# Kernel optimization log

Measured on AMD Instinct MI355X. Metric: run time of the kernel, lower is better.

The kernel has to match this reference:

```python
import jax, jax.numpy as jnp
import numpy as np

B, N, C, H, W = 4, 262144, 40, 256, 256
HID = 128


def _bilinear_sample(plane, u, v):
    """torch F.grid_sample(mode='bilinear', padding_mode='zeros', align_corners=False).
    plane: (B, C, H, W); u, v: (B, N) in [-1, 1] (u -> width axis, v -> height axis).
    Returns (B, N, C)."""
    Wd, Hd = plane.shape[3], plane.shape[2]
    ix = ((u + 1.0) * Wd - 1.0) * 0.5
    iy = ((v + 1.0) * Hd - 1.0) * 0.5
    ix0 = jnp.floor(ix)
    iy0 = jnp.floor(iy)
    fx = ix - ix0
    fy = iy - iy0
    ix0 = ix0.astype(jnp.int32)
    iy0 = iy0.astype(jnp.int32)
    flat = plane.reshape(plane.shape[0], plane.shape[1], Hd * Wd)  # (B,C,H*W)

    def corner(xi, yi, w):
        valid = (xi >= 0) & (xi < Wd) & (yi >= 0) & (yi < Hd)
        xc = jnp.clip(xi, 0, Wd - 1)
        yc = jnp.clip(yi, 0, Hd - 1)
        idx = yc * Wd + xc  # (B,N)
        vals = jnp.take_along_axis(flat, idx[:, None, :], axis=2)  # (B,C,N)
        return vals * (w * valid)[:, None, :]

    out = (corner(ix0, iy0, (1 - fx) * (1 - fy))
           + corner(ix0 + 1, iy0, fx * (1 - fy))
           + corner(ix0, iy0 + 1, (1 - fx) * fy)
           + corner(ix0 + 1, iy0 + 1, fx * fy))  # (B,C,N)
    return jnp.transpose(out, (0, 2, 1))  # (B,N,C)


def _sample_triplane(triplane, coords):
    x, y, z = coords[..., 0], coords[..., 1], coords[..., 2]
    f_xy = _bilinear_sample(triplane[:, 0], x, y)
    f_xz = _bilinear_sample(triplane[:, 1], x, z)
    f_yz = _bilinear_sample(triplane[:, 2], y, z)
    return jnp.concatenate([f_xy, f_xz, f_yz], axis=-1)  # (B,N,3C)


def setup_inputs() -> dict:
    key = jax.random.key(0)
    ks = jax.random.split(key, 16)
    triplane = jax.random.normal(ks[0], (B, 3, C, H, W), dtype=jnp.float32)
    coords = jax.random.uniform(ks[1], (B, N, 3), dtype=jnp.float32) * 2.0 - 1.0
    vd = jax.random.normal(ks[2], (B, N, 3), dtype=jnp.float32)
    view_dirs = vd / (jnp.linalg.norm(vd, axis=-1, keepdims=True) + 1e-8)
    s = 0.05
    p = {
        'triplane': triplane, 'coords': coords, 'view_dirs': view_dirs,
        'dw1': jax.random.normal(ks[3], (3 * C, HID), dtype=jnp.float32) * s,
        'db1': jnp.zeros((HID,), jnp.float32),
        'dw2': jax.random.normal(ks[4], (HID, HID), dtype=jnp.float32) * s,
        'db2': jnp.zeros((HID,), jnp.float32),
        'dw3': jax.random.normal(ks[5], (HID, 1), dtype=jnp.float32) * s,
        'db3': jnp.zeros((1,), jnp.float32),
        'cw1': jax.random.normal(ks[6], (3 * C + 3, HID), dtype=jnp.float32) * s,
        'cb1': jnp.zeros((HID,), jnp.float32),
        'cw2': jax.random.normal(ks[7], (HID, HID), dtype=jnp.float32) * s,
        'cb2': jnp.zeros((HID,), jnp.float32),
        'cw3': jax.random.normal(ks[8], (HID, 3), dtype=jnp.float32) * s,
        'cb3': jnp.zeros((3,), jnp.float32),
    }
    return p


def reference(triplane, coords, view_dirs, dw1, db1, dw2, db2, dw3, db3,
              cw1, cb1, cw2, cb2, cw3, cb3):
    feats = _sample_triplane(triplane, coords)  # (B,N,3C)
    h = jax.nn.relu(feats @ dw1 + db1)
    h = jax.nn.relu(h @ dw2 + db2)
    density = h @ dw3 + db3  # (B,N,1)
    cin = jnp.concatenate([feats, view_dirs], axis=-1)
    g = jax.nn.relu(cin @ cw1 + cb1)
    g = jax.nn.relu(g @ cw2 + cb2)
    rgb = jax.nn.sigmoid(g @ cw3 + cb3)  # (B,N,3)
    return density, rgb
```

## Files before the change

kernel.cpp:

```cpp
#include <hip/hip_runtime.h>
#include <cstdint>
#include <cstddef>

typedef __bf16 bf16x8 __attribute__((ext_vector_type(8)));
typedef float  f32x4  __attribute__((ext_vector_type(4)));

#define MFMA16(a,b,c) __builtin_amdgcn_mfma_f32_16x16x32_bf16((a),(b),(c),0,0,0)

__device__ __forceinline__ uint f2bf1(float f){
  uint u = __builtin_bit_cast(uint, f);
  u += 0x7FFFu + ((u >> 16) & 1u);
  return u >> 16;
}
__device__ __forceinline__ uint pack2(float a, float b){
  return f2bf1(a) | (f2bf1(b) << 16);
}
__device__ __forceinline__ uint pack2f(float a, float b){
  uint ua = __builtin_bit_cast(uint, a) + 0x8000u;
  uint ub = __builtin_bit_cast(uint, b) + 0x8000u;
  return __builtin_amdgcn_perm(ub, ua, 0x07060302u);
}
__device__ __forceinline__ float bflo(uint d){ return __builtin_bit_cast(float, d << 16); }
__device__ __forceinline__ float bfhi(uint d){ return __builtin_bit_cast(float, d & 0xFFFF0000u); }

__global__ __launch_bounds__(256, 4) void prep_k(
    const float* __restrict__ tri, ushort* __restrict__ tp,
    const float* __restrict__ dw1, const float* __restrict__ cw1,
    const float* __restrict__ dw2, const float* __restrict__ cw2,
    const float* __restrict__ dw3, const float* __restrict__ cw3,
    uint4* __restrict__ wpk)
{
  __shared__ ushort st[64 * 41];
  const int tid = threadIdx.x;
  if (blockIdx.x < 12288){
    const int bi  = blockIdx.x;
    const int xb  = bi & 3;
    const int y   = (bi >> 2) & 255;
    const int q   = bi >> 10;
    const float* src = tri + (size_t)q * 40 * 65536 + y * 256 + xb * 64;
#pragma unroll
    for (int it = 0; it < 10; it++){
      int lin = it * 256 + tid;
      int c = lin >> 6, x = lin & 63;
      float v = src[(size_t)c * 65536 + x];
      st[x * 41 + c] = (ushort)f2bf1(v);
    }
    __syncthreads();
    uint* dst = (uint*)(tp + ((size_t)q * 65536 + (size_t)y * 256 + xb * 64) * 40);
#pragma unroll
    for (int it = 0; it < 5; it++){
      int lin = it * 256 + tid;
      int e  = lin * 2;
      int x1 = (e * 1639) >> 16;       int c1 = e  - x1 * 40;
      int e2 = e + 1;
      int x2 = (e2 * 1639) >> 16;      int c2 = e2 - x2 * 40;
      dst[lin] = (uint)st[x1 * 41 + c1] | ((uint)st[x2 * 41 + c2] << 16);
    }
  } else {
    int idx = (blockIdx.x - 12288) * 256 + tid;
    if (idx >= 8704) return;
    int mode, rel;
    if      (idx < 2048){ mode = 0; rel = idx; }
    else if (idx < 4096){ mode = 1; rel = idx - 2048; }
    else if (idx < 6144){ mode = 2; rel = idx - 4096; }
    else if (idx < 8192){ mode = 3; rel = idx - 6144; }
    else if (idx < 8448){ mode = 4; rel = idx - 8192; }
    else                { mode = 5; rel = idx - 8448; }
    int frag = rel >> 6, lane = rel & 63;
    int Mt = frag >> 2, s = frag & 3;
    int m  = Mt * 16 + (lane & 15);
    int kb = s * 32 + (lane >> 4) * 8;
    uint d[4];
#pragma unroll
    for (int jj = 0; jj < 4; jj++){
      float v0 = 0.f, v1 = 0.f;
#pragma unroll
      for (int h = 0; h < 2; h++){
        int k = kb + jj * 2 + h;
        float v = 0.f;
        switch (mode){
          case 0: v = (k < 120) ? dw1[k * 128 + m] : 0.f; break;
          case 1: v = (k < 123) ? cw1[k * 128 + m] : 0.f; break;
          case 2: v = dw2[k * 128 + m]; break;
          case 3: v = cw2[k * 128 + m]; break;
          case 4: v = (m == 0) ? dw3[k] : 0.f; break;
          default: v = (m >= 1 && m <= 3) ? cw3[k * 3 + (m - 1)] : 0.f; break;
        }
        if (h == 0) v0 = v; else v1 = v;
      }
      d[jj] = pack2(v0, v1);
    }
    uint4 o; o.x = d[0]; o.y = d[1]; o.z = d[2]; o.w = d[3];
    wpk[idx] = o;
  }
}

__device__ __forceinline__ void stage_w(const uint4* __restrict__ g,
                                        uint4* l, int wave, int lane, int n){
  const int chunks = n >> 6;
  for (int c = wave; c < chunks; c += 8){
    __builtin_amdgcn_global_load_lds(
      (const __attribute__((address_space(1))) void*)(g + c * 64 + lane),
      (__attribute__((address_space(3))) void*)(l + c * 64 + lane),
      16, 0, 0);
  }
}

__device__ __forceinline__ uint4 blend4(uint4 a, uint4 b, uint4 c, uint4 d,
                                        float w00, float w10, float w01, float w11){
  uint4 ov;
  ov.x = pack2f(w00*bflo(a.x)+w10*bflo(b.x)+w01*bflo(c.x)+w11*bflo(d.x),
                w00*bfhi(a.x)+w10*bfhi(b.x)+w01*bfhi(c.x)+w11*bfhi(d.x));
  ov.y = pack2f(w00*bflo(a.y)+w10*bflo(b.y)+w01*bflo(c.y)+w11*bflo(d.y),
                w00*bfhi(a.y)+w10*bfhi(b.y)+w01*bfhi(c.y)+w11*bfhi(d.y));
  ov.z = pack2f(w00*bflo(a.z)+w10*bflo(b.z)+w01*bflo(c.z)+w11*bflo(d.z),
                w00*bfhi(a.z)+w10*bfhi(b.z)+w01*bfhi(c.z)+w11*bfhi(d.z));
  ov.w = pack2f(w00*bflo(a.w)+w10*bflo(b.w)+w01*bflo(c.w)+w11*bflo(d.w),
                w00*bfhi(a.w)+w10*bfhi(b.w)+w01*bfhi(c.w)+w11*bfhi(d.w));
  return ov;
}

__device__ __forceinline__ bf16x8 read_h(const uint* S, int s, int t, int lrow, int lq){
  int dwb = (s * 16 + lq * 4 + (lrow << 2)) & 63;
  return __builtin_bit_cast(bf16x8, *(const uint4*)&S[(t * 16 + lrow) * 64 + dwb]);
}

__device__ __forceinline__ void put_h(uint* S, f32x4 v, int Mt, int t, int lrow, int lq){
  uint2 w;
  w.x = pack2f(fmaxf(v[0], 0.f), fmaxf(v[1], 0.f));
  w.y = pack2f(fmaxf(v[2], 0.f), fmaxf(v[3], 0.f));
  int dw = (Mt * 8 + lq * 2 + (lrow << 2)) & 63;
  *(uint2*)&S[(t * 16 + lrow) * 64 + dw] = w;
}

__device__ __forceinline__ void layer1(uint* S, const uint4* W,
                                       const float* __restrict__ bias,
                                       const uint4 (&bf)[4][2],
                                       int lrow, int lq, int lane){
  f32x4 acc[8][2];
#pragma unroll
  for (int Mt = 0; Mt < 8; Mt++){
    f32x4 bi = *(const f32x4*)(bias + Mt * 16 + lq * 4);
    acc[Mt][0] = bi; acc[Mt][1] = bi;
  }
#pragma unroll
  for (int s = 0; s < 4; s++)
#pragma unroll
    for (int Mt = 0; Mt < 8; Mt++){
      bf16x8 aw = __builtin_bit_cast(bf16x8, W[(Mt * 4 + s) * 64 + lane]);
      acc[Mt][0] = MFMA16(aw, __builtin_bit_cast(bf16x8, bf[s][0]), acc[Mt][0]);
      acc[Mt][1] = MFMA16(aw, __builtin_bit_cast(bf16x8, bf[s][1]), acc[Mt][1]);
    }
#pragma unroll
  for (int Mt = 0; Mt < 8; Mt++){
    put_h(S, acc[Mt][0], Mt, 0, lrow, lq);
    put_h(S, acc[Mt][1], Mt, 1, lrow, lq);
  }
}

__device__ __forceinline__ void dense_l(uint* S, const uint4* W,
                                        const float* __restrict__ bias,
                                        int lrow, int lq, int lane){
  f32x4 acc[8][2];
#pragma unroll
  for (int Mt = 0; Mt < 8; Mt++){
    f32x4 bi = *(const f32x4*)(bias + Mt * 16 + lq * 4);
    acc[Mt][0] = bi; acc[Mt][1] = bi;
  }
#pragma unroll
  for (int s = 0; s < 4; s++){
    bf16x8 bh0 = read_h(S, s, 0, lrow, lq);
    bf16x8 bh1 = read_h(S, s, 1, lrow, lq);
#pragma unroll
    for (int Mt = 0; Mt < 8; Mt++){
      bf16x8 aw = __builtin_bit_cast(bf16x8, W[(Mt * 4 + s) * 64 + lane]);
      acc[Mt][0] = MFMA16(aw, bh0, acc[Mt][0]);
      acc[Mt][1] = MFMA16(aw, bh1, acc[Mt][1]);
    }
  }
#pragma unroll
  for (int Mt = 0; Mt < 8; Mt++){
    put_h(S, acc[Mt][0], Mt, 0, lrow, lq);
    put_h(S, acc[Mt][1], Mt, 1, lrow, lq);
  }
}

__device__ __forceinline__ void out_l(const uint* S, const uint4* W,
                                      f32x4 (&acc3)[2], int lrow, int lq, int lane){
#pragma unroll
  for (int s = 0; s < 4; s++){
    bf16x8 aw = __builtin_bit_cast(bf16x8, W[s * 64 + lane]);
    acc3[0] = MFMA16(aw, read_h(S, s, 0, lrow, lq), acc3[0]);
    acc3[1] = MFMA16(aw, read_h(S, s, 1, lrow, lq), acc3[1]);
  }
}

__global__ __launch_bounds__(512, 2) void fused_k(
    const ushort* __restrict__ tp, const float* __restrict__ coords,
    const float* __restrict__ vdirs, const uint4* __restrict__ wpk,
    const float* __restrict__ db1, const float* __restrict__ db2,
    const float* __restrict__ db3, const float* __restrict__ cb1,
    const float* __restrict__ cb2, const float* __restrict__ cb3,
    float* __restrict__ out)
{
  extern __shared__ uint4 smem[];
  const int wave = threadIdx.x >> 6;
  uint*  S   = (uint*)(smem + (size_t)wave * 512);
  uint4* WB0 = smem + 4096;
  uint4* WB1 = smem + 6144;
  const int lane = threadIdx.x & 63, lrow = lane & 15, lq = lane >> 4;
  const int blk   = blockIdx.x;
  const int pbase = (blk & 3) * 262144 + (blk >> 2) * 256 + wave * 32;

  stage_w(wpk + 0, WB0, wave, lane, 2048);

  uint4 bf[4][2];
#pragma unroll
  for (int t = 0; t < 2; t++){
    const int p  = pbase + t * 16 + lrow;
    const int bb = p >> 18;
    const float cx = coords[3 * p], cy = coords[3 * p + 1], cz = coords[3 * p + 2];
    float pw00[3], pw10[3], pw01[3], pw11[3];
    uint  o00[3], o10[3], o01[3], o11[3];
#pragma unroll
    for (int pl = 0; pl < 3; pl++){
      const float u = (pl == 2) ? cy : cx;
      const float v = (pl == 0) ? cy : cz;
      float ix = fmaf(u, 128.f, 127.5f);
      float iy = fmaf(v, 128.f, 127.5f);
      float fx0 = floorf(ix), fy0 = floorf(iy);
      float fx = ix - fx0, fy = iy - fy0;
      int x0 = (int)fx0, y0 = (int)fy0;
      float wx0 = (x0 >= 0  && x0 < 256) ? (1.f - fx) : 0.f;
      float wx1 = (x0 >= -1 && x0 < 255) ? fx : 0.f;
      float wy0 = (y0 >= 0  && y0 < 256) ? (1.f - fy) : 0.f;
      float wy1 = (y0 >= -1 && y0 < 255) ? fy : 0.f;
      int xc0 = min(max(x0, 0), 255), xc1 = min(max(x0 + 1, 0), 255);
      int yc0 = min(max(y0, 0), 255), yc1 = min(max(y0 + 1, 0), 255);
      pw00[pl] = wx0 * wy0; pw10[pl] = wx1 * wy0;
      pw01[pl] = wx0 * wy1; pw11[pl] = wx1 * wy1;
      o00[pl] = ((uint)yc0 * 256u + (uint)xc0) * 40u;
      o10[pl] = ((uint)yc0 * 256u + (uint)xc1) * 40u;
      o01[pl] = ((uint)yc1 * 256u + (uint)xc0) * 40u;
      o11[pl] = ((uint)yc1 * 256u + (uint)xc1) * 40u;
    }
#pragma unroll
    for (int s = 0; s < 4; s++){
      const int chunk = s * 4 + lq;
      if (chunk == 15){
        const float v0 = vdirs[3 * p], v1 = vdirs[3 * p + 1], v2 = vdirs[3 * p + 2];
        uint4 tt; tt.x = pack2f(v0, v1); tt.y = pack2f(v2, 0.f); tt.z = 0u; tt.w = 0u;
        bf[s][t] = tt;
      } else {
        const int pl = (chunk < 5) ? 0 : (chunk < 10) ? 1 : 2;
        const int c0 = chunk * 8 - pl * 40;
        const ushort* base = tp + (size_t)(bb * 3 + pl) * 2621440 + c0;
        uint4 a = *(const uint4*)(base + o00[pl]);
        uint4 b = *(const uint4*)(base + o10[pl]);
        uint4 c = *(const uint4*)(base + o01[pl]);
        uint4 d = *(const uint4*)(base + o11[pl]);
        bf[s][t] = blend4(a, b, c, d, pw00[pl], pw10[pl], pw01[pl], pw11[pl]);
      }
    }
  }

  f32x4 acc3[2];
  {
    float i0 = (lq == 0) ? db3[0] : 0.f;
    float i1 = (lq == 0) ? cb3[0] : 0.f;
    float i2 = (lq == 0) ? cb3[1] : 0.f;
    float i3 = (lq == 0) ? cb3[2] : 0.f;
    f32x4 iv = {i0, i1, i2, i3};
    acc3[0] = iv; acc3[1] = iv;
  }

  __syncthreads();

  stage_w(wpk + 4096, WB1, wave, lane, 2048);
  layer1 (S, WB0, db1, bf, lrow, lq, lane);
  __syncthreads();

  stage_w(wpk + 8192, WB0, wave, lane, 256);
  dense_l(S, WB1, db2, lrow, lq, lane);
  __syncthreads();

  stage_w(wpk + 2048, WB1, wave, lane, 2048);
  out_l  (S, WB0, acc3, lrow, lq, lane);
  __syncthreads();

  stage_w(wpk + 6144, WB0, wave, lane, 2048);
  layer1 (S, WB1, cb1, bf, lrow, lq, lane);
  __syncthreads();

  stage_w(wpk + 8448, WB1, wave, lane, 256);
  dense_l(S, WB0, cb2, lrow, lq, lane);
  __syncthreads();

  out_l  (S, WB1, acc3, lrow, lq, lane);

  if (lq == 0){
#pragma unroll
    for (int t = 0; t < 2; t++){
      int p = pbase + t * 16 + lrow;
      out[p] = acc3[t][0];
      float* rgb = out + 1048576 + (size_t)p * 3;
      rgb[0] = 1.f / (1.f + __expf(-acc3[t][1]));
      rgb[1] = 1.f / (1.f + __expf(-acc3[t][2]));
      rgb[2] = 1.f / (1.f + __expf(-acc3[t][3]));
    }
  }
}

extern "C" void kernel_launch(void* const* d_in, const int* in_sizes, int n_in,
                              void* d_out, int out_size, void* d_ws, size_t ws_size,
                              hipStream_t stream)
{
  (void)in_sizes; (void)n_in; (void)out_size; (void)ws_size;
  const float* tri    = (const float*)d_in[0];
  const float* coords = (const float*)d_in[1];
  const float* vdirs  = (const float*)d_in[2];
  const float* dw1 = (const float*)d_in[3];  const float* db1 = (const float*)d_in[4];
  const float* dw2 = (const float*)d_in[5];  const float* db2 = (const float*)d_in[6];
  const float* dw3 = (const float*)d_in[7];  const float* db3 = (const float*)d_in[8];
  const float* cw1 = (const float*)d_in[9];  const float* cb1 = (const float*)d_in[10];
  const float* cw2 = (const float*)d_in[11]; const float* cb2 = (const float*)d_in[12];
  const float* cw3 = (const float*)d_in[13]; const float* cb3 = (const float*)d_in[14];

  char* ws = (char*)d_ws;
  const size_t planes_bytes = 62914560;
  ushort* tp  = (ushort*)ws;
  uint4*  wpk = (uint4*)(ws + planes_bytes);

  (void)hipFuncSetAttribute((const void*)fused_k,
                            hipFuncAttributeMaxDynamicSharedMemorySize, 131072);

  prep_k<<<12322, 256, 0, stream>>>(tri, tp, dw1, cw1, dw2, cw2, dw3, cw3, wpk);
  fused_k<<<4096, 512, 131072, stream>>>(tp, coords, vdirs, wpk,
                                         db1, db2, db3, cb1, cb2, cb3,
                                         (float*)d_out);
}
```

Measured before the change: 643.2 us.

## Read MLP weights directly from global memory and drop LDS weight staging

The fused kernel no longer stages weight fragments into LDS with block-wide barriers between layers. Each wave now reads packed weights straight from global memory, which should be cache-resident, and keeps only a small per-wave static LDS scratch. That frees shared memory and removes syncs, so the launch bound moves to 4 blocks of 512 threads for higher occupancy. Separately, the prep transpose loads four channels per thread and writes 8-byte packed LDS and global stores. The risks are heavier VMEM/L2 traffic for the weight fragments and register pressure under the tighter launch bound.

Result: slower. 804.0 us (+25.0%).

```diff
diff --git a/kernel.cpp b/kernel.cpp
--- a/kernel.cpp
+++ b/kernel.cpp
@@ -30,7 +30,7 @@
     const float* __restrict__ dw3, const float* __restrict__ cw3,
     uint4* __restrict__ wpk)
 {
-  __shared__ ushort st[64 * 41];
+  __shared__ ushort st[64 * 44];
   const int tid = threadIdx.x;
   if (blockIdx.x < 12288){
     const int bi  = blockIdx.x;
@@ -39,22 +39,29 @@
     const int q   = bi >> 10;
     const float* src = tri + (size_t)q * 40 * 65536 + y * 256 + xb * 64;
 #pragma unroll
-    for (int it = 0; it < 10; it++){
+    for (int it = 0; it < 3; it++){
       int lin = it * 256 + tid;
-      int c = lin >> 6, x = lin & 63;
-      float v = src[(size_t)c * 65536 + x];
-      st[x * 41 + c] = (ushort)f2bf1(v);
+      if (lin < 640){
+        int x = lin & 63, cg = lin >> 6;
+        float v0 = src[(size_t)(cg * 4 + 0) * 65536 + x];
+        float v1 = src[(size_t)(cg * 4 + 1) * 65536 + x];
+        float v2 = src[(size_t)(cg * 4 + 2) * 65536 + x];
+        float v3 = src[(size_t)(cg * 4 + 3) * 65536 + x];
+        uint2 w; w.x = pack2(v0, v1); w.y = pack2(v2, v3);
+        *(uint2*)&st[x * 44 + cg * 4] = w;
+      }
     }
     __syncthreads();
     uint* dst = (uint*)(tp + ((size_t)q * 65536 + (size_t)y * 256 + xb * 64) * 40);
 #pragma unroll
-    for (int it = 0; it < 5; it++){
-      int lin = it * 256 + tid;
-      int e  = lin * 2;
-      int x1 = (e * 1639) >> 16;       int c1 = e  - x1 * 40;
-      int e2 = e + 1;
-      int x2 = (e2 * 1639) >> 16;      int c2 = e2 - x2 * 40;
-      dst[lin] = (uint)st[x1 * 41 + c1] | ((uint)st[x2 * 41 + c2] << 16);
+    for (int it = 0; it < 3; it++){
+      int m = it * 256 + tid;
+      if (m < 640){
+        int x  = (m * 6554) >> 16;
+        int jm = m - x * 10;
+        uint2 w = *(const uint2*)&st[x * 44 + jm * 4];
+        *(uint2*)&dst[2 * m] = w;
+      }
     }
   } else {
     int idx = (blockIdx.x - 12288) * 256 + tid;
@@ -95,17 +102,6 @@
   }
 }
 
-__device__ __forceinline__ void stage_w(const uint4* __restrict__ g,
-                                        uint4* l, int wave, int lane, int n){
-  const int chunks = n >> 6;
-  for (int c = wave; c < chunks; c += 8){
-    __builtin_amdgcn_global_load_lds(
-      (const __attribute__((address_space(1))) void*)(g + c * 64 + lane),
-      (__attribute__((address_space(3))) void*)(l + c * 64 + lane),
-      16, 0, 0);
-  }
-}
-
 __device__ __forceinline__ uint4 blend4(uint4 a, uint4 b, uint4 c, uint4 d,
                                         float w00, float w10, float w01, float w11){
   uint4 ov;
@@ -133,7 +129,7 @@
   *(uint2*)&S[(t * 16 + lrow) * 64 + dw] = w;
 }
 
-__device__ __forceinline__ void layer1(uint* S, const uint4* W,
+__device__ __forceinline__ void layer1(uint* S, const uint4* __restrict__ W,
                                        const float* __restrict__ bias,
                                        const uint4 (&bf)[4][2],
                                        int lrow, int lq, int lane){
@@ -158,7 +154,7 @@
   }
 }
 
-__device__ __forceinline__ void dense_l(uint* S, const uint4* W,
+__device__ __forceinline__ void dense_l(uint* S, const uint4* __restrict__ W,
                                         const float* __restrict__ bias,
                                         int lrow, int lq, int lane){
   f32x4 acc[8][2];
@@ -185,7 +181,7 @@
   }
 }
 
-__device__ __forceinline__ void out_l(const uint* S, const uint4* W,
+__device__ __forceinline__ void out_l(const uint* S, const uint4* __restrict__ W,
                                       f32x4 (&acc3)[2], int lrow, int lq, int lane){
 #pragma unroll
   for (int s = 0; s < 4; s++){
@@ -195,7 +191,7 @@
   }
 }
 
-__global__ __launch_bounds__(512, 2) void fused_k(
+__global__ __launch_bounds__(512, 4) void fused_k(
     const ushort* __restrict__ tp, const float* __restrict__ coords,
     const float* __restrict__ vdirs, const uint4* __restrict__ wpk,
     const float* __restrict__ db1, const float* __restrict__ db2,
@@ -203,16 +199,12 @@
     const float* __restrict__ cb2, const float* __restrict__ cb3,
     float* __restrict__ out)
 {
-  extern __shared__ uint4 smem[];
+  __shared__ uint smem[8][2048];
   const int wave = threadIdx.x >> 6;
-  uint*  S   = (uint*)(smem + (size_t)wave * 512);
-  uint4* WB0 = smem + 4096;
-  uint4* WB1 = smem + 6144;
+  uint* S = smem[wave];
   const int lane = threadIdx.x & 63, lrow = lane & 15, lq = lane >> 4;
   const int blk   = blockIdx.x;
   const int pbase = (blk & 3) * 262144 + (blk >> 2) * 256 + wave * 32;
-
-  stage_w(wpk + 0, WB0, wave, lane, 2048);
 
   uint4 bf[4][2];
 #pragma unroll
@@ -274,29 +266,12 @@
     acc3[0] = iv; acc3[1] = iv;
   }
 
-  __syncthreads();
-
-  stage_w(wpk + 4096, WB1, wave, lane, 2048);
-  layer1 (S, WB0, db1, bf, lrow, lq, lane);
-  __syncthreads();
-
-  stage_w(wpk + 8192, WB0, wave, lane, 256);
-  dense_l(S, WB1, db2, lrow, lq, lane);
-  __syncthreads();
-
-  stage_w(wpk + 2048, WB1, wave, lane, 2048);
-  out_l  (S, WB0, acc3, lrow, lq, lane);
-  __syncthreads();
-
-  stage_w(wpk + 6144, WB0, wave, lane, 2048);
-  layer1 (S, WB1, cb1, bf, lrow, lq, lane);
-  __syncthreads();
-
-  stage_w(wpk + 8448, WB1, wave, lane, 256);
-  dense_l(S, WB0, cb2, lrow, lq, lane);
-  __syncthreads();
-
-  out_l  (S, WB1, acc3, lrow, lq, lane);
+  layer1 (S, wpk,        db1, bf, lrow, lq, lane);
+  dense_l(S, wpk + 4096, db2,     lrow, lq, lane);
+  out_l  (S, wpk + 8192, acc3,    lrow, lq, lane);
+  layer1 (S, wpk + 2048, cb1, bf, lrow, lq, lane);
+  dense_l(S, wpk + 6144, cb2,     lrow, lq, lane);
+  out_l  (S, wpk + 8448, acc3,    lrow, lq, lane);
 
   if (lq == 0){
 #pragma unroll
@@ -331,11 +306,8 @@
   ushort* tp  = (ushort*)ws;
   uint4*  wpk = (uint4*)(ws + planes_bytes);
 
-  (void)hipFuncSetAttribute((const void*)fused_k,
-                            hipFuncAttributeMaxDynamicSharedMemorySize, 131072);
-
   prep_k<<<12322, 256, 0, stream>>>(tri, tp, dw1, cw1, dw2, cw2, dw3, cw3, wpk);
-  fused_k<<<4096, 512, 131072, stream>>>(tp, coords, vdirs, wpk,
-                                         db1, db2, db3, cb1, cb2, cb3,
-                                         (float*)d_out);
-}
+  fused_k<<<4096, 512, 0, stream>>>(tp, coords, vdirs, wpk,
+                                    db1, db2, db3, cb1, cb2, cb3,
+                                    (float*)d_out);
+}
```
